# Performance work log

Hardware: AMD Instinct MI355X
Metric: run time of the kernel (lower is better)

Reference implementation:

```python
import math
import jax, jax.numpy as jnp
import numpy as np

NUM_CODE = 4096
CODE_DIM = 256
IN_DIM = 1024

def chi_dist_mean_std(c):
    mean = math.sqrt(2.0) * math.exp(math.lgamma((c + 1) / 2) - math.lgamma(c / 2))
    std = math.sqrt(c - mean ** 2)
    return mean, std

MU, SIGMA = chi_dist_mean_std(CODE_DIM)


def setup_inputs() -> dict:
    key = jax.random.key(0)
    k1, k2, k3 = jax.random.split(key, 3)
    encode = jax.random.normal(k1, (8, 64, 64, CODE_DIM), dtype=jnp.float32)
    codebook_w = jax.random.normal(k2, (NUM_CODE, IN_DIM), dtype=jnp.float32)  # N(0,1) init
    proj_w = jax.random.normal(k3, (CODE_DIM, IN_DIM), dtype=jnp.float32) * (1.0 / math.sqrt(IN_DIM))
    proj_b = jnp.zeros((CODE_DIM,), dtype=jnp.float32)
    return {"encode": encode, "codebook_w": codebook_w, "proj_w": proj_w, "proj_b": proj_b}


def _cdist(z, e):
    # pairwise euclidean distance: [T, K]
    z2 = jnp.sum(z * z, axis=-1, keepdims=True)          # [T,1]
    e2 = jnp.sum(e * e, axis=-1)[None, :]                # [1,K]
    d2 = z2 + e2 - 2.0 * jnp.einsum('tc,kc->tk', z, e)
    return jnp.sqrt(jnp.maximum(d2, 0.0))


def reference(encode, codebook_w, proj_w, proj_b):
    b, h, w, c = encode.shape
    e = codebook_w @ proj_w.T + proj_b                   # [K, code_dim]
    z = encode.reshape(-1, c)                            # [T, code_dim]
    s = -_cdist(z, e)                                    # [T, K] (computed under no_grad in torch)
    simi = (s.reshape(b, h, w, -1) - MU) / SIGMA
    zsoft = jax.nn.softmax(simi, axis=-1)                # eval path (std=0)
    zidx = jnp.argmax(zsoft, axis=-1)                    # [b,h,w]
    quant = e[zidx]                                      # [b,h,w,code_dim]
    return (zidx, quant)
```

## Files before the change

kernel.cpp:

```cpp
#include <hip/hip_runtime.h>
#include <hip/hip_bf16.h>


#define K_CODES 4096
#define CDIM    256
#define IDIM    1024
#define NTOK    32768

typedef __attribute__((ext_vector_type(8))) short short8;
typedef __attribute__((ext_vector_type(4))) float f32x4;

__device__ __forceinline__ unsigned short f32_to_bf16_rne(float f) {
  union { float f; unsigned int u; } x; x.f = f;
  unsigned int r = x.u + 0x7FFFu + ((x.u >> 16) & 1u);
  return (unsigned short)(r >> 16);
}
__device__ __forceinline__ float bf16_to_f32(unsigned short h) {
  union { unsigned int u; float f; } x; x.u = ((unsigned int)h) << 16;
  return x.f;
}

extern "C" __global__ __launch_bounds__(256)
void proj_gemm(const float* __restrict__ cb, const float* __restrict__ pw,
               const float* __restrict__ pb, float* __restrict__ e,
               unsigned short* __restrict__ Ect) {
  __shared__ float As[32][68];
  __shared__ float Bs[32][68];
  const int tid = threadIdx.x;
  const int tx = tid & 15, ty = tid >> 4;
  const int m0 = blockIdx.y << 6;
  const int n0 = blockIdx.x << 6;
  const int r  = tid >> 2;
  const int c8 = (tid & 3) << 3;
  float acc[4][4] = {};
  for (int k0 = 0; k0 < IDIM; k0 += 32) {
    float4 a0 = *(const float4*)&cb[(m0 + r) * IDIM + k0 + c8];
    float4 a1 = *(const float4*)&cb[(m0 + r) * IDIM + k0 + c8 + 4];
    float4 b0 = *(const float4*)&pw[(n0 + r) * IDIM + k0 + c8];
    float4 b1 = *(const float4*)&pw[(n0 + r) * IDIM + k0 + c8 + 4];
    __syncthreads();
    As[c8+0][r]=a0.x; As[c8+1][r]=a0.y; As[c8+2][r]=a0.z; As[c8+3][r]=a0.w;
    As[c8+4][r]=a1.x; As[c8+5][r]=a1.y; As[c8+6][r]=a1.z; As[c8+7][r]=a1.w;
    Bs[c8+0][r]=b0.x; Bs[c8+1][r]=b0.y; Bs[c8+2][r]=b0.z; Bs[c8+3][r]=b0.w;
    Bs[c8+4][r]=b1.x; Bs[c8+5][r]=b1.y; Bs[c8+6][r]=b1.z; Bs[c8+7][r]=b1.w;
    __syncthreads();
    #pragma unroll
    for (int kk = 0; kk < 32; ++kk) {
      const float4 av = *(const float4*)&As[kk][ty*4];
      const float4 bv = *(const float4*)&Bs[kk][tx*4];
      const float a4[4] = {av.x, av.y, av.z, av.w};
      const float b4[4] = {bv.x, bv.y, bv.z, bv.w};
      #pragma unroll
      for (int i = 0; i < 4; ++i)
        #pragma unroll
        for (int j = 0; j < 4; ++j)
          acc[i][j] += a4[i] * b4[j];
    }
  }
  const int col0 = n0 + tx*4;
  const int kb   = col0 >> 5;
  const int g    = (col0 >> 3) & 3;
  const int half = (col0 >> 2) & 1;
  #pragma unroll
  for (int i = 0; i < 4; ++i) {
    const int row = m0 + ty*4 + i;
    float vv[4];
    unsigned short h4[4], l4[4];
    #pragma unroll
    for (int j = 0; j < 4; ++j) {
      vv[j] = acc[i][j] + pb[col0 + j];
      h4[j] = f32_to_bf16_rne(vv[j]);
      l4[j] = f32_to_bf16_rne(vv[j] - bf16_to_f32(h4[j]));
    }
    *(float4*)&e[(size_t)row * CDIM + col0] = *(float4*)vv;
    const int ct = row >> 4, cl = row & 15;
    const size_t fi = ((size_t)(kb      * 256 + ct) * 64 + g*16 + cl) * 8 + half*4;
    const size_t fo = ((size_t)((kb+8)  * 256 + ct) * 64 + g*16 + cl) * 8 + half*4;
    *(ushort4*)&Ect[fi] = *(ushort4*)h4;
    *(ushort4*)&Ect[fo] = *(ushort4*)l4;
  }
}

extern "C" __global__ __launch_bounds__(256)
void compute_e2(const float* __restrict__ e, float* __restrict__ e2) {
  const int gid  = blockIdx.x * 256 + threadIdx.x;
  const int w    = gid >> 6;
  const int lane = threadIdx.x & 63;
  float4 v = *(const float4*)&e[(size_t)w * CDIM + (lane << 2)];
  float s = v.x*v.x + v.y*v.y + v.z*v.z + v.w*v.w;
  #pragma unroll
  for (int off = 32; off > 0; off >>= 1) s += __shfl_down(s, off, 64);
  if (lane == 0) e2[w] = s;
}

extern "C" __global__ __launch_bounds__(512, 2)
void score_mfma(const float* __restrict__ z, const unsigned short* __restrict__ Ect,
                const float* __restrict__ e2g, const float* __restrict__ eg,
                float* __restrict__ zidx_f, float* __restrict__ quant) {
  extern __shared__ __align__(16) char smem[];
  char* Zb = smem;

  const int tid = threadIdx.x;
  const int l   = tid & 63;
  const int w   = tid >> 6;
  const int t0  = blockIdx.x << 6;

  {
    const int r  = tid >> 3;
    const int cq = tid & 7;
    const int i4 = r >> 4;
    const int rl = (r & 15) << 4;
    #pragma unroll
    for (int it = 0; it < 4; ++it) {
      const int col = cq*32 + it*8;
      const float4 v0 = *(const float4*)&z[(size_t)(t0 + r) * CDIM + col];
      const float4 v1 = *(const float4*)&z[(size_t)(t0 + r) * CDIM + col + 4];
      float vv[8] = {v0.x,v0.y,v0.z,v0.w,v1.x,v1.y,v1.z,v1.w};
      unsigned int hp[4], lp[4];
      #pragma unroll
      for (int c = 0; c < 4; ++c) {
        unsigned short h0 = f32_to_bf16_rne(vv[2*c]);
        unsigned short h1 = f32_to_bf16_rne(vv[2*c+1]);
        unsigned short l0 = f32_to_bf16_rne(vv[2*c]   - bf16_to_f32(h0));
        unsigned short l1 = f32_to_bf16_rne(vv[2*c+1] - bf16_to_f32(h1));
        hp[c] = (unsigned int)h0 | ((unsigned int)h1 << 16);
        lp[c] = (unsigned int)l0 | ((unsigned int)l1 << 16);
      }
      const int lane_b = it*256 + rl;
      *(uint4*)(Zb + (size_t)(i4*16 + cq    ) * 1024 + lane_b) = *(uint4*)hp;
      *(uint4*)(Zb + (size_t)(i4*16 + cq + 8) * 1024 + lane_b) = *(uint4*)lp;
    }
  }
  __syncthreads();

  float bestv[4][4];
  int   besti[4][4];
  #pragma unroll
  for (int i = 0; i < 4; ++i)
    #pragma unroll
    for (int r = 0; r < 4; ++r) { bestv[i][r] = 3.4e38f; besti[i][r] = 0; }

  const int cl = l & 15;
  const int g  = l >> 4;

  const char* ebase = (const char*)Ect + (size_t)l * 16 + (size_t)w * 4096;
  const char* Zl    = Zb + (size_t)l * 16;

  short8 aHc[4], aLc[4], bHc[4], bLc[4];
  #pragma unroll
  for (int i = 0; i < 4; ++i) {
    aHc[i] = *(const short8*)(Zl + (size_t)(i*16 + 0) * 1024);
    aLc[i] = *(const short8*)(Zl + (size_t)(i*16 + 8) * 1024);
  }
  #pragma unroll
  for (int jj = 0; jj < 4; ++jj) {
    bHc[jj] = *(const short8*)(ebase + (size_t)0 * 262144 + jj * 1024);
    bLc[jj] = *(const short8*)(ebase + (size_t)8 * 262144 + jj * 1024);
  }

  for (int cc = 0; cc < 8; ++cc) {
    const char* ecc  = ebase + (size_t)cc * 32768;
    const char* eccn = ebase + (size_t)((cc + 1) & 7) * 32768;

    f32x4 acc[4][4];
    #pragma unroll
    for (int i = 0; i < 4; ++i)
      #pragma unroll
      for (int jj = 0; jj < 4; ++jj) acc[i][jj] = (f32x4){0.f,0.f,0.f,0.f};

    float e2v[4];
    #pragma unroll
    for (int jj = 0; jj < 4; ++jj)
      e2v[jj] = e2g[cc*512 + w*64 + jj*16 + cl];

    #pragma unroll
    for (int kw = 0; kw < 8; ++kw) {
      short8 aHn[4], aLn[4], bHn[4], bLn[4];
      {
        const char* bsrc = (kw < 7) ? ecc : eccn;
        const int kwn = (kw + 1) & 7;
        #pragma unroll
        for (int jj = 0; jj < 4; ++jj) {
          bHn[jj] = *(const short8*)(bsrc + (size_t)(kwn    ) * 262144 + jj * 1024);
          bLn[jj] = *(const short8*)(bsrc + (size_t)(kwn + 8) * 262144 + jj * 1024);
        }
        #pragma unroll
        for (int i = 0; i < 4; ++i) {
          aHn[i] = *(const short8*)(Zl + (size_t)(i*16 + kwn    ) * 1024);
          aLn[i] = *(const short8*)(Zl + (size_t)(i*16 + kwn + 8) * 1024);
        }
      }
      __builtin_amdgcn_s_setprio(1);
      #pragma unroll
      for (int i = 0; i < 4; ++i)
        #pragma unroll
        for (int jj = 0; jj < 4; ++jj)
          acc[i][jj] = __builtin_amdgcn_mfma_f32_16x16x32_bf16(aHc[i], bHc[jj], acc[i][jj], 0, 0, 0);
      #pragma unroll
      for (int i = 0; i < 4; ++i)
        #pragma unroll
        for (int jj = 0; jj < 4; ++jj)
          acc[i][jj] = __builtin_amdgcn_mfma_f32_16x16x32_bf16(aHc[i], bLc[jj], acc[i][jj], 0, 0, 0);
      #pragma unroll
      for (int i = 0; i < 4; ++i)
        #pragma unroll
        for (int jj = 0; jj < 4; ++jj)
          acc[i][jj] = __builtin_amdgcn_mfma_f32_16x16x32_bf16(aLc[i], bHc[jj], acc[i][jj], 0, 0, 0);
      __builtin_amdgcn_s_setprio(0);
      #pragma unroll
      for (int i = 0; i < 4; ++i) { aHc[i] = aHn[i]; aLc[i] = aLn[i]; }
      #pragma unroll
      for (int jj = 0; jj < 4; ++jj) { bHc[jj] = bHn[jj]; bLc[jj] = bLn[jj]; }
    }
    #pragma unroll
    for (int jj = 0; jj < 4; ++jj) {
      const int code = cc*512 + w*64 + jj*16 + cl;
      #pragma unroll
      for (int i = 0; i < 4; ++i)
        #pragma unroll
        for (int r = 0; r < 4; ++r) {
          const float sc = e2v[jj] - 2.0f * acc[i][jj][r];
          if (sc < bestv[i][r]) { bestv[i][r] = sc; besti[i][r] = code; }
        }
    }
  }

  struct RP { float v; int i; };
  RP*  red    = (RP*)(smem + 65536);
  int* sh_idx = (int*)(smem + 65536 + 4096);
  #pragma unroll
  for (int i = 0; i < 4; ++i)
    #pragma unroll
    for (int r = 0; r < 4; ++r) {
      float v = bestv[i][r]; int bi = besti[i][r];
      #pragma unroll
      for (int m = 1; m < 16; m <<= 1) {
        const float ov = __shfl_xor(v, m, 64);
        const int   oi = __shfl_xor(bi, m, 64);
        if (ov < v || (ov == v && oi < bi)) { v = ov; bi = oi; }
      }
      if (cl == 0) {
        const int tl = i*16 + g*4 + r;
        red[tl*8 + w].v = v; red[tl*8 + w].i = bi;
      }
    }
  __syncthreads();
  if (tid < 64) {
    float v = red[tid*8].v; int bi = red[tid*8].i;
    #pragma unroll
    for (int x = 1; x < 8; ++x) {
      const float ov = red[tid*8 + x].v; const int oi = red[tid*8 + x].i;
      if (ov < v || (ov == v && oi < bi)) { v = ov; bi = oi; }
    }
    zidx_f[t0 + tid] = (float)bi;
    sh_idx[tid] = bi;
  }
  __syncthreads();

  {
    const int r   = tid >> 3;
    const int cq  = (tid & 7) << 5;
    const int idx = sh_idx[r];
    #pragma unroll
    for (int it = 0; it < 4; ++it) {
      const float4 v0 = *(const float4*)&eg[(size_t)idx * CDIM + cq + it*8];
      const float4 v1 = *(const float4*)&eg[(size_t)idx * CDIM + cq + it*8 + 4];
      *(float4*)&quant[(size_t)(t0 + r) * CDIM + cq + it*8]     = v0;
      *(float4*)&quant[(size_t)(t0 + r) * CDIM + cq + it*8 + 4] = v1;
    }
  }
}

extern "C" void kernel_launch(void* const* d_in, const int* in_sizes, int n_in,
                              void* d_out, int out_size, void* d_ws, size_t ws_size,
                              hipStream_t stream) {
  const float* encode = (const float*)d_in[0];
  const float* cb     = (const float*)d_in[1];
  const float* pw     = (const float*)d_in[2];
  const float* pb     = (const float*)d_in[3];

  float* e  = (float*)d_ws;
  float* e2 = e + (size_t)K_CODES * CDIM;
  unsigned short* Ect = (unsigned short*)(e2 + K_CODES);

  float* out     = (float*)d_out;
  float* zidx_f  = out;
  float* quant_f = out + NTOK;

  (void)hipFuncSetAttribute((const void*)score_mfma,
                            hipFuncAttributeMaxDynamicSharedMemorySize, 70912);

  proj_gemm<<<dim3(CDIM/64, K_CODES/64), 256, 0, stream>>>(cb, pw, pb, e, Ect);
  compute_e2<<<(K_CODES*64)/256, 256, 0, stream>>>(e, e2);
  score_mfma<<<NTOK/64, 512, 70912, stream>>>(encode, Ect, e2, e, zidx_f, quant_f);
}
```

Measured before the change: 229.0 us.

## Process 128 tokens per block with 2x4 warp split over tokens and codes

```diff
diff --git a/kernel.cpp b/kernel.cpp
--- a/kernel.cpp
+++ b/kernel.cpp
@@ -103,12 +103,15 @@
   const int tid = threadIdx.x;
   const int l   = tid & 63;
   const int w   = tid >> 6;
-  const int t0  = blockIdx.x << 6;
-
-  {
-    const int r  = tid >> 3;
+  const int tg  = w >> 2;
+  const int cg  = w & 3;
+  const int t0  = blockIdx.x << 7;
+
+  #pragma unroll
+  for (int rr = 0; rr < 2; ++rr) {
+    const int r  = rr*64 + (tid >> 3);
     const int cq = tid & 7;
-    const int i4 = r >> 4;
+    const int i8 = r >> 4;
     const int rl = (r & 15) << 4;
     #pragma unroll
     for (int it = 0; it < 4; ++it) {
@@ -127,8 +130,8 @@
         lp[c] = (unsigned int)l0 | ((unsigned int)l1 << 16);
       }
       const int lane_b = it*256 + rl;
-      *(uint4*)(Zb + (size_t)(i4*16 + cq    ) * 1024 + lane_b) = *(uint4*)hp;
-      *(uint4*)(Zb + (size_t)(i4*16 + cq + 8) * 1024 + lane_b) = *(uint4*)lp;
+      *(uint4*)(Zb + (size_t)(i8*16 + cq    ) * 1024 + lane_b) = *(uint4*)hp;
+      *(uint4*)(Zb + (size_t)(i8*16 + cq + 8) * 1024 + lane_b) = *(uint4*)lp;
     }
   }
   __syncthreads();
@@ -143,8 +146,8 @@
   const int cl = l & 15;
   const int g  = l >> 4;
 
-  const char* ebase = (const char*)Ect + (size_t)l * 16 + (size_t)w * 4096;
-  const char* Zl    = Zb + (size_t)l * 16;
+  const char* ebase = (const char*)Ect + (size_t)l * 16 + (size_t)cg * 4096;
+  const char* Zl    = Zb + (size_t)l * 16 + (size_t)tg * 65536;
 
   short8 aHc[4], aLc[4], bHc[4], bLc[4];
   #pragma unroll
@@ -158,9 +161,9 @@
     bLc[jj] = *(const short8*)(ebase + (size_t)8 * 262144 + jj * 1024);
   }
 
-  for (int cc = 0; cc < 8; ++cc) {
-    const char* ecc  = ebase + (size_t)cc * 32768;
-    const char* eccn = ebase + (size_t)((cc + 1) & 7) * 32768;
+  for (int cc = 0; cc < 16; ++cc) {
+    const char* ecc  = ebase + (size_t)cc * 16384;
+    const char* eccn = ebase + (size_t)((cc + 1) & 15) * 16384;
 
     f32x4 acc[4][4];
     #pragma unroll
@@ -171,7 +174,7 @@
     float e2v[4];
     #pragma unroll
     for (int jj = 0; jj < 4; ++jj)
-      e2v[jj] = e2g[cc*512 + w*64 + jj*16 + cl];
+      e2v[jj] = e2g[cc*256 + cg*64 + jj*16 + cl];
 
     #pragma unroll
     for (int kw = 0; kw < 8; ++kw) {
@@ -214,7 +217,7 @@
     }
     #pragma unroll
     for (int jj = 0; jj < 4; ++jj) {
-      const int code = cc*512 + w*64 + jj*16 + cl;
+      const int code = cc*256 + cg*64 + jj*16 + cl;
       #pragma unroll
       for (int i = 0; i < 4; ++i)
         #pragma unroll
@@ -226,8 +229,8 @@
   }
 
   struct RP { float v; int i; };
-  RP*  red    = (RP*)(smem + 65536);
-  int* sh_idx = (int*)(smem + 65536 + 4096);
+  RP*  red    = (RP*)(smem + 131072);
+  int* sh_idx = (int*)(smem + 131072 + 4096);
   #pragma unroll
   for (int i = 0; i < 4; ++i)
     #pragma unroll
@@ -240,16 +243,16 @@
         if (ov < v || (ov == v && oi < bi)) { v = ov; bi = oi; }
       }
       if (cl == 0) {
-        const int tl = i*16 + g*4 + r;
-        red[tl*8 + w].v = v; red[tl*8 + w].i = bi;
+        const int tl = tg*64 + i*16 + g*4 + r;
+        red[tl*4 + cg].v = v; red[tl*4 + cg].i = bi;
       }
     }
   __syncthreads();
-  if (tid < 64) {
-    float v = red[tid*8].v; int bi = red[tid*8].i;
-    #pragma unroll
-    for (int x = 1; x < 8; ++x) {
-      const float ov = red[tid*8 + x].v; const int oi = red[tid*8 + x].i;
+  if (tid < 128) {
+    float v = red[tid*4].v; int bi = red[tid*4].i;
+    #pragma unroll
+    for (int x = 1; x < 4; ++x) {
+      const float ov = red[tid*4 + x].v; const int oi = red[tid*4 + x].i;
       if (ov < v || (ov == v && oi < bi)) { v = ov; bi = oi; }
     }
     zidx_f[t0 + tid] = (float)bi;
@@ -257,8 +260,9 @@
   }
   __syncthreads();
 
-  {
-    const int r   = tid >> 3;
+  #pragma unroll
+  for (int rr = 0; rr < 2; ++rr) {
+    const int r   = rr*64 + (tid >> 3);
     const int cq  = (tid & 7) << 5;
     const int idx = sh_idx[r];
     #pragma unroll
@@ -288,9 +292,9 @@
   float* quant_f = out + NTOK;
 
   (void)hipFuncSetAttribute((const void*)score_mfma,
-                            hipFuncAttributeMaxDynamicSharedMemorySize, 70912);
+                            hipFuncAttributeMaxDynamicSharedMemorySize, 135680);
 
   proj_gemm<<<dim3(CDIM/64, K_CODES/64), 256, 0, stream>>>(cb, pw, pb, e, Ect);
   compute_e2<<<(K_CODES*64)/256, 256, 0, stream>>>(e, e2);
-  score_mfma<<<NTOK/64, 512, 70912, stream>>>(encode, Ect, e2, e, zidx_f, quant_f);
-}
+  score_mfma<<<NTOK/128, 512, 135680, stream>>>(encode, Ect, e2, e, zidx_f, quant_f);
+}
```

After: 222.6 us. -2.8%, faster.
